# Performance work log

Hardware: AMD Instinct MI355X
Metric: run time of the kernel (lower is better)

Reference implementation:

```python
import math
import jax, jax.numpy as jnp
import numpy as np

B, NP = 256, 3
LAT, TXT, D = 512, 768, 768
NL = 6
DI, DS, DC = 2 * D, 16, 4
DTR = math.ceil(D / 16)
EPS = 1e-5


def _silu(x):
    return x * jax.nn.sigmoid(x)


def _layernorm(x, g, b):
    m = x.mean(-1, keepdims=True)
    v = ((x - m) ** 2).mean(-1, keepdims=True)
    return (x - m) / jnp.sqrt(v + EPS) * g + b


def _mamba(x, in_w, conv_w, conv_b, xproj_w, dt_w, dt_b, Alog, Dp, out_w):
    # x: [B, L, D]; standard Mamba(d_state=16, d_conv=4, expand=2)
    Bb, L, _ = x.shape
    xz = jnp.einsum('bld,ed->ble', x, in_w)          # [B, L, 2*DI]
    u, z = jnp.split(xz, 2, axis=-1)
    # depthwise causal conv (kernel DC, left pad DC-1, truncated to L)
    up = jnp.pad(u, ((0, 0), (DC - 1, 0), (0, 0)))
    uc = conv_b + sum(conv_w[:, k] * up[:, k:k + L, :] for k in range(DC))
    uc = _silu(uc)
    xdbl = jnp.einsum('bld,ed->ble', uc, xproj_w)    # [B, L, DTR+2*DS]
    dt, Bm, Cm = jnp.split(xdbl, [DTR, DTR + DS], axis=-1)
    dt = jax.nn.softplus(jnp.einsum('blr,dr->bld', dt, dt_w) + dt_b)  # [B,L,DI]
    A = -jnp.exp(Alog)                               # [DI, DS]

    def step(h, xs):
        dt_t, B_t, C_t, u_t = xs                     # [B,DI],[B,DS],[B,DS],[B,DI]
        dA = jnp.exp(dt_t[..., None] * A)            # [B,DI,DS]
        h = h * dA + (dt_t * u_t)[..., None] * B_t[:, None, :]
        y = jnp.einsum('bds,bs->bd', h, C_t)
        return h, y

    h0 = jnp.zeros((Bb, DI, DS), x.dtype)
    xs = (dt.transpose(1, 0, 2), Bm.transpose(1, 0, 2),
          Cm.transpose(1, 0, 2), uc.transpose(1, 0, 2))
    _, ys = jax.lax.scan(step, h0, xs)
    y = ys.transpose(1, 0, 2) + Dp * uc
    y = y * _silu(z)
    return jnp.einsum('bld,ed->ble', y, out_w)       # [B, L, D]


def _forward(z_noisy, timestep, text_emb,
             zin_w, zin_b, tin_w, tin_b, time_w, time_b, part_emb,
             local_w, local_b, f_w, f_b, fuse_w, fuse_b, final_w, final_b,
             ln_g, ln_b, m_in_w, m_conv_w, m_conv_b, m_xproj_w, m_dt_w,
             m_dt_b, m_Alog, m_Dp, m_out_w, oln_g, oln_b, zout_w, zout_b):
    z_feat = jnp.einsum('bpl,dl->bpd', z_noisy, zin_w) + zin_b + part_emb
    text_feat = (text_emb @ tin_w.T + tin_b)[:, None]            # [B,1,D]
    half = D // 2
    freqs = jnp.exp(-math.log(10000.0) * jnp.arange(half, dtype=jnp.float32) / half)
    targ = timestep.astype(jnp.float32)[:, None] * freqs
    temb = jnp.concatenate([jnp.cos(targ), jnp.sin(targ)], -1)   # [B,D]
    time_feat = (temb @ time_w.T + time_b)[:, None]              # [B,1,D]
    x = jnp.concatenate([time_feat, text_feat, z_feat], 1)       # [B,5,D]
    # sinusoidal position embedding (first 5 rows of max_len=10 table)
    pos = jnp.arange(5, dtype=jnp.float32)[:, None]
    div = jnp.exp(jnp.arange(0, D, 2, dtype=jnp.float32) * (-math.log(10000.0) / D))
    pe = jnp.zeros((5, D), jnp.float32)
    pe = pe.at[:, 0::2].set(jnp.sin(pos * div)).at[:, 1::2].set(jnp.cos(pos * div))
    x = x + pe[None]
    text_cond = x[:, 1, :]                                       # [B,D]
    for i in range(NL):
        residual = x
        xl = _silu(jnp.einsum('bld,ed->ble', x, local_w[i]) + local_b[i])
        y_rep = jnp.broadcast_to(text_cond[:, None, :], xl.shape)
        yhat = jnp.einsum('bld,ed->ble', jnp.concatenate([xl, y_rep], -1), f_w[i]) + f_b[i]
        y_gate = y_rep * jax.nn.sigmoid(yhat)
        xt = jnp.einsum('bld,ed->ble', jnp.concatenate([xl, y_gate], -1), fuse_w[i]) + fuse_b[i]
        mf = lambda v, d: _mamba(v, m_in_w[i, d], m_conv_w[i, d], m_conv_b[i, d],
                                 m_xproj_w[i, d], m_dt_w[i, d], m_dt_b[i, d],
                                 m_Alog[i, d], m_Dp[i, d], m_out_w[i, d])
        xf = mf(xt, 0)
        xb = jnp.flip(mf(jnp.flip(xt, 1), 1), 1)
        xo = jnp.einsum('bld,ed->ble', jnp.concatenate([xf, xb], -1), final_w[i]) + final_b[i]
        x = _layernorm(xo + residual, ln_g[i], ln_b[i])
    z_out = x[:, 2:, :]                                          # [B,3,D]
    return jnp.einsum('bpd,ld->bpl', _layernorm(z_out, oln_g, oln_b), zout_w) + zout_b


def setup_inputs() -> dict:
    key = jax.random.key(0)
    kit = iter(jax.random.split(key, 40))

    def rn(shape, s=0.02):
        return jax.random.normal(next(kit), shape, jnp.float32) * s

    inp = dict(
        z_noisy=jax.random.normal(next(kit), (B, NP, LAT), jnp.float32),
        text_emb=jax.random.normal(next(kit), (B, TXT), jnp.float32),
        zin_w=rn((D, LAT)), zin_b=jnp.zeros((D,), jnp.float32),
        tin_w=rn((D, TXT)), tin_b=jnp.zeros((D,), jnp.float32),
        time_w=rn((D, D)), time_b=jnp.zeros((D,), jnp.float32),
        part_emb=rn((1, NP, D)),
        local_w=rn((NL, D, D)), local_b=jnp.zeros((NL, D), jnp.float32),
        f_w=rn((NL, D, 2 * D)), f_b=jnp.zeros((NL, D), jnp.float32),
        fuse_w=rn((NL, D, 2 * D)), fuse_b=jnp.zeros((NL, D), jnp.float32),
        final_w=rn((NL, D, 2 * D)), final_b=jnp.zeros((NL, D), jnp.float32),
        ln_g=jnp.ones((NL, D), jnp.float32), ln_b=jnp.zeros((NL, D), jnp.float32),
        m_in_w=rn((NL, 2, 2 * DI, D)),
        m_conv_w=rn((NL, 2, DI, DC), 0.1),
        m_conv_b=jnp.zeros((NL, 2, DI), jnp.float32),
        m_xproj_w=rn((NL, 2, DTR + 2 * DS, DI)),
        m_dt_w=rn((NL, 2, DI, DTR), 0.1),
        m_dt_b=jnp.full((NL, 2, DI), -4.6, jnp.float32),
        m_Alog=jnp.tile(jnp.log(jnp.arange(1, DS + 1, dtype=jnp.float32)), (NL, 2, DI, 1)),
        m_Dp=jnp.ones((NL, 2, DI), jnp.float32),
        m_out_w=rn((NL, 2, D, DI)),
        oln_g=jnp.ones((D,), jnp.float32), oln_b=jnp.zeros((D,), jnp.float32),
        zout_w=rn((LAT, D)), zout_b=jnp.zeros((LAT,), jnp.float32),
        timestep=jax.random.randint(next(kit), (B,), 0, 1000),
    )
    return inp


def reference(z_noisy, text_emb, zin_w, zin_b, tin_w, tin_b, time_w, time_b,
              part_emb, local_w, local_b, f_w, f_b, fuse_w, fuse_b, final_w,
              final_b, ln_g, ln_b, m_in_w, m_conv_w, m_conv_b, m_xproj_w,
              m_dt_w, m_dt_b, m_Alog, m_Dp, m_out_w, oln_g, oln_b, zout_w,
              zout_b, timestep):
    return _forward(z_noisy, timestep, text_emb, zin_w, zin_b, tin_w, tin_b,
                    time_w, time_b, part_emb, local_w, local_b, f_w, f_b,
                    fuse_w, fuse_b, final_w, final_b, ln_g, ln_b, m_in_w,
                    m_conv_w, m_conv_b, m_xproj_w, m_dt_w, m_dt_b, m_Alog,
                    m_Dp, m_out_w, oln_g, oln_b, zout_w, zout_b)
```

## Files before the change

### kernel.cpp

```cpp
#include <hip/hip_runtime.h>
#include <hip/hip_bf16.h>
#include <math.h>

#define B_   256
#define NP_  3
#define LAT_ 512
#define TXT_ 768
#define D_   768
#define NL_  6
#define DI_  1536
#define DS_  16
#define DC_  4
#define DTR_ 48
#define L_   5
#define M_   (B_*L_)
#define EPS_ 1e-5f

#define OB_WBF    0ull
#define OB_XPP    139591680ull
#define OB_TEMB   144310272ull
#define OB_ZNORM  144703488ull
#define OB_XBF    145883136ull
#define OB_TCBF   147849216ull
#define OB_CAT1   148242432ull
#define OB_XTBF   152174592ull
#define OB_XZBF   154140672ull
#define OB_UCY    169869312ull
#define OB_CAT2   177733632ull
#define OB_X      181665792ull
#define OB_TC     185597952ull
#define OB_TCF    186384384ull
#define OB_ZFEAT  187170816ull
#define OB_XO     189530112ull
#define OB_PART   193462272ull

#define WO_LOCAL  0u
#define WO_F      3538944u
#define WO_FUSE   10616832u
#define WO_FINAL  17694720u
#define WO_IN     24772608u
#define WO_OUT    53084160u
#define WO_ZIN    67239936u
#define WO_TIN    67633152u
#define WO_TIME   68222976u
#define WO_ZOUT   68812800u
#define WO_ZNOISY 69206016u
#define WO_TEXT   69599232u
#define WO_END    69795840u

#define CVT_BLOCKS  17040u
#define XPAD_BLOCKS 1152u
#define TEMB_BLOCKS 384u
#define PREP_BLOCKS (CVT_BLOCKS + XPAD_BLOCKS + TEMB_BLOCKS)

typedef __attribute__((ext_vector_type(4))) float floatx4;
typedef __attribute__((ext_vector_type(8))) short short8;
typedef __attribute__((ext_vector_type(8))) unsigned short ushort8v;
typedef __attribute__((ext_vector_type(4))) unsigned short ushort4v;

__device__ __forceinline__ float sigm(float v) { return 1.f / (1.f + expf(-v)); }
__device__ __forceinline__ float softplus(float v) {
    return fmaxf(v, 0.f) + log1pf(expf(-fabsf(v)));
}
__device__ __forceinline__ unsigned short bf16rn(float f) {
    unsigned int u = __builtin_bit_cast(unsigned int, f);
    u = (u + 0x7fffu + ((u >> 16) & 1u)) >> 16;
    return (unsigned short)u;
}
__device__ __forceinline__ float b2f(unsigned short u) {
    unsigned int x = ((unsigned int)u) << 16;
    return __builtin_bit_cast(float, x);
}

template<int N> __device__ __forceinline__ void waitv() {
    asm volatile("s_waitcnt vmcnt(%0)" :: "i"(N) : "memory");
}

struct CvtArgs { const float* s[12]; };

__global__ __launch_bounds__(256) void prep_kernel(
    CvtArgs a, unsigned short* __restrict__ dst,
    const float* __restrict__ xw, unsigned short* __restrict__ xpd,
    const int* __restrict__ ts, unsigned short* __restrict__ temb)
{
    unsigned bid = blockIdx.x;
    if (bid < CVT_BLOCKS) {
        constexpr unsigned ends[12] = {
            3538944u, 10616832u, 17694720u, 24772608u, 53084160u, 67239936u,
            67633152u, 68222976u, 68812800u, 69206016u, 69599232u, 69795840u };
        const unsigned wv = (bid * 256u + threadIdx.x) >> 6;
        const unsigned lane = threadIdx.x & 63u;
        const unsigned wbase = wv * 1024u;
        if (wbase >= WO_END) return;
#pragma unroll
        for (int q = 0; q < 4; ++q) {
            unsigned gbase = wbase + (unsigned)q * 256u;
            if (gbase >= WO_END) return;
            int t = 0;
            while (gbase >= ends[t]) ++t;
            unsigned start = t ? ends[t - 1] : 0u;
            unsigned idx = gbase + lane * 4u;
            floatx4 v = __builtin_nontemporal_load((const floatx4*)(a.s[t] + (idx - start)));
            ushort4v o = { bf16rn(v[0]), bf16rn(v[1]), bf16rn(v[2]), bf16rn(v[3]) };
            __builtin_nontemporal_store(o, (ushort4v*)(dst + idx));
        }
    } else if (bid < CVT_BLOCKS + XPAD_BLOCKS) {
        unsigned i8 = ((bid - CVT_BLOCKS) * 256u + threadIdx.x) * 8u;
        if (i8 >= 12u * 128u * 1536u) return;
        unsigned pi = i8 / (128u * 1536u);
        unsigned rem = i8 - pi * 128u * 1536u;
        unsigned row = rem / 1536u, col = rem - row * 1536u;
        ushort8v o = {0, 0, 0, 0, 0, 0, 0, 0};
        if (row < 80u) {
            const float* s = xw + ((size_t)pi * 80u + row) * 1536u + col;
            floatx4 v0 = __builtin_nontemporal_load((const floatx4*)s);
            floatx4 v1 = __builtin_nontemporal_load((const floatx4*)(s + 4));
            o = ushort8v{ bf16rn(v0[0]), bf16rn(v0[1]), bf16rn(v0[2]), bf16rn(v0[3]),
                          bf16rn(v1[0]), bf16rn(v1[1]), bf16rn(v1[2]), bf16rn(v1[3]) };
        }
        *(ushort8v*)(xpd + i8) = o;
    } else {
        int idx = (bid - CVT_BLOCKS - XPAD_BLOCKS) * 256 + threadIdx.x;
        if (idx >= B_ * 384) return;
        int j = idx % 384, b = idx / 384;
        float f = expf(-logf(10000.f) * (float)j / 384.f);
        float targ = (float)ts[b] * f;
        temb[(size_t)b * D_ + j]       = bf16rn(cosf(targ));
        temb[(size_t)b * D_ + 384 + j] = bf16rn(sinf(targ));
    }
}

template<int BM, int BN, int CD, int DEPTH, int PF>
__global__ __launch_bounds__(256) void gemm_bf16_kernel(
    const unsigned short* __restrict__ A, int lda,
    const unsigned short* __restrict__ W, int wld,
    const float* __restrict__ bias,
    const float* __restrict__ aux0,
    const float* __restrict__ aux1,
    void* __restrict__ Cv, int ldc,
    int M, int N, int K, int epi, int ncap,
    int zsplit, unsigned long long zA, unsigned long long zW, unsigned long long zC)
{
    constexpr int GA = BM / 64;
    constexpr int GB = BN / 64;
    constexpr int LPS = GA + GB;
    constexpr int FRM = BM / 32;
    constexpr int FRN = BN / 32;
    constexpr int BMSK = DEPTH - 1;

    const int z = blockIdx.z;
    const int dirz = z / zsplit, ksz = z - dirz * zsplit;
    A += (unsigned long long)dirz * zA + (unsigned long long)ksz * (unsigned)K;
    W += (unsigned long long)dirz * zW + (unsigned long long)ksz * (unsigned)K;

    __shared__ unsigned short lds[DEPTH][(BM + BN) * 32];

    const int tid = threadIdx.x;
    const int m0 = blockIdx.y * BM, n0 = blockIdx.x * BN;
    const int w = tid >> 6, lane = tid & 63;
    const int wr = w >> 1, wc = w & 1;
    const int lrow = lane & 15;
    const int lk = (lane >> 4) << 3;

    const int rA = tid >> 2, sA = tid & 3;
    const int scA = ((sA ^ ((rA >> 1) & 3)) << 3);
    floatx4 acc[FRM][FRN] = {};

    auto stage = [&](int buf, int k0) {
        unsigned short* base = &lds[buf][0];
#pragma unroll
        for (int i = 0; i < GA; ++i) {
            int t = tid + i * 256;
            int r = t >> 2;
            const unsigned short* src = A + (size_t)(m0 + r) * lda + k0 + scA;
            __builtin_amdgcn_global_load_lds(
                (const __attribute__((address_space(1))) unsigned int*)(const void*)src,
                (__attribute__((address_space(3))) unsigned int*)(void*)(base + i * 2048 + w * 512),
                16, 0, 0);
        }
#pragma unroll
        for (int i = 0; i < GB; ++i) {
            int t = tid + i * 256;
            int r = t >> 2;
            const unsigned short* src = W + (size_t)(n0 + r) * wld + k0 + scA;
            __builtin_amdgcn_global_load_lds(
                (const __attribute__((address_space(1))) unsigned int*)(const void*)src,
                (__attribute__((address_space(3))) unsigned int*)(void*)(base + BM * 32 + i * 2048 + w * 512),
                16, 0, 0);
        }
    };

    const int nt = K >> 5;
#pragma unroll
    for (int s = 0; s < PF; ++s)
        if (s < nt) stage(s, s << 5);

    int offA[FRM], offB[FRN];
#pragma unroll
    for (int i = 0; i < FRM; ++i) {
        int row = wr * (BM / 2) + i * 16 + lrow;
        offA[i] = row * 32 + (lk ^ (((row >> 1) & 3) << 3));
    }
#pragma unroll
    for (int j = 0; j < FRN; ++j) {
        int row = wc * (BN / 2) + j * 16 + lrow;
        offB[j] = BM * 32 + row * 32 + (lk ^ (((row >> 1) & 3) << 3));
    }

    for (int t = 0; t < nt; ++t) {
        int rem = nt - 1 - t;
        if (rem >= PF) { stage((t + PF) & BMSK, (t + PF) << 5); waitv<PF * LPS>(); }
        else if (rem == 5) waitv<5 * LPS>();
        else if (rem == 4) waitv<4 * LPS>();
        else if (rem == 3) waitv<3 * LPS>();
        else if (rem == 2) waitv<2 * LPS>();
        else if (rem == 1) waitv<1 * LPS>();
        else               waitv<0>();
        __builtin_amdgcn_s_barrier();
        const unsigned short* pl = &lds[t & BMSK][0];
        short8 af[FRM], bfv[FRN];
#pragma unroll
        for (int i = 0; i < FRM; ++i) af[i] = *(const short8*)(pl + offA[i]);
#pragma unroll
        for (int j = 0; j < FRN; ++j) bfv[j] = *(const short8*)(pl + offB[j]);
#pragma unroll
        for (int i = 0; i < FRM; ++i)
#pragma unroll
            for (int j = 0; j < FRN; ++j)
                acc[i][j] = __builtin_amdgcn_mfma_f32_16x16x32_bf16(af[i], bfv[j], acc[i][j], 0, 0, 0);
    }

#pragma unroll
    for (int i = 0; i < FRM; ++i) {
        int row0 = m0 + wr * (BM / 2) + i * 16 + (lane >> 4) * 4;
#pragma unroll
        for (int j = 0; j < FRN; ++j) {
            int col = n0 + wc * (BN / 2) + j * 16 + lrow;
            if (col >= ncap) continue;
            float bb = bias ? bias[col] : 0.f;
#pragma unroll
            for (int r = 0; r < 4; ++r) {
                int row = row0 + r;
                float v = acc[i][j][r] + bb;
                if (epi == 1) {
                    v = v * sigm(v);
                } else if (epi == 3) {
                    int b = row / 5;
                    v = acc[i][j][r] + bb + b2f(((const unsigned short*)aux0)[(size_t)b * 768 + col]);
                    v = aux1[(size_t)b * 768 + col] * sigm(v);
                }
                size_t off = (size_t)z * zC + (size_t)row * ldc + col;
                if (CD == 1) ((float*)Cv)[off] = v;
                else         ((unsigned short*)Cv)[off] = bf16rn(v);
            }
        }
    }
}

__global__ void finalize_embed_kernel(float* __restrict__ x,
                                      unsigned short* __restrict__ xbf,
                                      const float* __restrict__ zfeat,
                                      const float* __restrict__ part_emb,
                                      float* __restrict__ tc,
                                      unsigned short* __restrict__ tcbf)
{
    int idx = blockIdx.x * blockDim.x + threadIdx.x;
    if (idx >= B_ * L_ * D_) return;
    int d = idx % D_;
    int bl = idx / D_;
    int l = bl % L_, b = bl / L_;
    float v;
    if (l >= 2) v = zfeat[((size_t)(b * 3 + (l - 2))) * D_ + d] + part_emb[(size_t)(l - 2) * D_ + d];
    else        v = x[idx];
    int j = d >> 1;
    float dv = expf((float)(2 * j) * (-logf(10000.f) / (float)D_));
    float ang = (float)l * dv;
    v += (d & 1) ? cosf(ang) : sinf(ang);
    x[idx] = v;
    xbf[idx] = bf16rn(v);
    if (l == 1) { tc[(size_t)b * D_ + d] = v; tcbf[(size_t)b * D_ + d] = bf16rn(v); }
}

__global__ __launch_bounds__(256) void conv_silu_kernel(
    const unsigned short* __restrict__ xz,
    const float* __restrict__ cw,
    const float* __restrict__ cb,
    unsigned short* __restrict__ ucy)
{
    int idx = blockIdx.x * 256 + threadIdx.x;
    if (idx >= 2 * M_ * DI_ / 8) return;
    int c8 = (idx % (DI_ / 8)) * 8;
    int t2 = idx / (DI_ / 8);
    int bl = t2 % M_, dir = t2 / M_;
    int l = bl % L_, b = bl / L_;

    float acc[8];
    const float* cbp = cb + dir * DI_ + c8;
#pragma unroll
    for (int e = 0; e < 8; ++e) acc[e] = cbp[e];
    floatx4 w[8];
#pragma unroll
    for (int e = 0; e < 8; ++e)
        w[e] = *(const floatx4*)(cw + ((size_t)(dir * DI_ + c8 + e)) * DC_);
#pragma unroll
    for (int k = 0; k < DC_; ++k) {
        int lp = dir ? (l + 3 - k) : (l + k - 3);
        if (lp >= 0 && lp < L_) {
            ushort8v xv = *(const ushort8v*)(xz + ((size_t)(b * L_ + lp)) * 6144 + dir * 3072 + c8);
#pragma unroll
            for (int e = 0; e < 8; ++e) acc[e] = fmaf(w[e][k], b2f(xv[e]), acc[e]);
        }
    }
    ushort8v o;
#pragma unroll
    for (int e = 0; e < 8; ++e) { float v = acc[e]; o[e] = bf16rn(v * sigm(v)); }
    *(ushort8v*)(ucy + (size_t)idx * 8) = o;
}

__global__ __launch_bounds__(256) void dtscan_kernel(
    const float* __restrict__ part,
    unsigned short* ucy,
    const unsigned short* __restrict__ xz,
    const float* __restrict__ dt_w,
    const float* __restrict__ dt_b,
    const float* __restrict__ Alog,
    const float* __restrict__ Dp)
{
    __shared__ float xd[L_][80];
    const int dir = blockIdx.z;
    const int b = blockIdx.y;
    const int ch = blockIdx.x * 256 + threadIdx.x;

    for (int o = threadIdx.x; o < L_ * 80; o += 256) {
        int l = o / 80, n = o - l * 80;
        float s = 0.f;
#pragma unroll
        for (int ks = 0; ks < 8; ++ks)
            s += part[((size_t)(dir * 8 + ks) * M_ + b * L_ + l) * 80 + n];
        xd[l][n] = s;
    }
    __syncthreads();

    const int cg = dir * DI_ + ch;
    float dt[L_];
    const float* wp = dt_w + (size_t)cg * DTR_;
    float dbv = dt_b[cg];
#pragma unroll
    for (int l = 0; l < L_; ++l) {
        float v = dbv;
#pragma unroll
        for (int r = 0; r < DTR_; ++r) v = fmaf(xd[l][r], wp[r], v);
        dt[l] = softplus(v);
    }

    float Aa[DS_], h[DS_];
#pragma unroll
    for (int s = 0; s < DS_; ++s) { Aa[s] = -expf(Alog[(size_t)cg * DS_ + s]); h[s] = 0.f; }
    float Dv = Dp[cg];

#pragma unroll
    for (int t = 0; t < L_; ++t) {
        const int l = dir ? (L_ - 1 - t) : t;
        size_t base = (size_t)(b * L_ + l);
        size_t uoff = ((size_t)dir * M_ + base) * DI_ + ch;
        float dtv = dt[l];
        float ucv = b2f(ucy[uoff]);
        float du = dtv * ucv;
        float y = 0.f;
#pragma unroll
        for (int s = 0; s < DS_; ++s) {
            h[s] = h[s] * expf(dtv * Aa[s]) + du * xd[l][48 + s];
            y = fmaf(h[s], xd[l][64 + s], y);
        }
        float zv = b2f(xz[base * 6144 + dir * 3072 + 1536 + ch]);
        ucy[uoff] = bf16rn((y + Dv * ucv) * (zv * sigm(zv)));
    }
}

__device__ __forceinline__ float block_sum(float v)
{
    __shared__ float sd[4];
#pragma unroll
    for (int o = 1; o < 64; o <<= 1) v += __shfl_xor(v, o, 64);
    int lane = threadIdx.x & 63, wid = threadIdx.x >> 6;
    if (lane == 0) sd[wid] = v;
    __syncthreads();
    v = sd[0] + sd[1] + sd[2] + sd[3];
    __syncthreads();
    return v;
}

__global__ __launch_bounds__(256) void ln_residual_kernel(
    const float* __restrict__ xo, float* __restrict__ x,
    unsigned short* __restrict__ xbf,
    const float* __restrict__ g, const float* __restrict__ bt,
    const float* __restrict__ og, const float* __restrict__ ob,
    unsigned short* __restrict__ znorm, int do_out)
{
    int row = blockIdx.x;
    const float* pa = xo + (size_t)row * D_;
    float* px = x + (size_t)row * D_;
    float v[3];
    float s = 0.f;
#pragma unroll
    for (int i = 0; i < 3; ++i) { int d = threadIdx.x + 256 * i; v[i] = pa[d] + px[d]; s += v[i]; }
    float mean = block_sum(s) * (1.f / (float)D_);
    float sq = 0.f;
#pragma unroll
    for (int i = 0; i < 3; ++i) { float t = v[i] - mean; sq += t * t; }
    float var = block_sum(sq) * (1.f / (float)D_);
    float inv = rsqrtf(var + EPS_);
    float o[3];
#pragma unroll
    for (int i = 0; i < 3; ++i) {
        int d = threadIdx.x + 256 * i;
        o[i] = (v[i] - mean) * inv * g[d] + bt[d];
        px[d] = o[i];
        xbf[(size_t)row * D_ + d] = bf16rn(o[i]);
    }
    int l = row % L_;
    if (do_out && l >= 2) {
        int b = row / L_;
        float s2 = o[0] + o[1] + o[2];
        float mean2 = block_sum(s2) * (1.f / (float)D_);
        float sq2 = 0.f;
#pragma unroll
        for (int i = 0; i < 3; ++i) { float t = o[i] - mean2; sq2 += t * t; }
        float var2 = block_sum(sq2) * (1.f / (float)D_);
        float inv2 = rsqrtf(var2 + EPS_);
#pragma unroll
        for (int i = 0; i < 3; ++i) {
            int d = threadIdx.x + 256 * i;
            znorm[((size_t)(b * 3 + (l - 2))) * D_ + d] = bf16rn((o[i] - mean2) * inv2 * og[d] + ob[d]);
        }
    }
}

extern "C" void kernel_launch(void* const* d_in, const int* in_sizes, int n_in,
                              void* d_out, int out_size, void* d_ws, size_t ws_size,
                              hipStream_t stream)
{
    const float* z_noisy  = (const float*)d_in[0];
    const float* text_emb = (const float*)d_in[1];
    const float* zin_b    = (const float*)d_in[3];
    const float* tin_b    = (const float*)d_in[5];
    const float* time_b   = (const float*)d_in[7];
    const float* part_emb = (const float*)d_in[8];
    const float* local_b  = (const float*)d_in[10];
    const float* f_b      = (const float*)d_in[12];
    const float* fuse_b   = (const float*)d_in[14];
    const float* final_b  = (const float*)d_in[16];
    const float* ln_g     = (const float*)d_in[17];
    const float* ln_b     = (const float*)d_in[18];
    const float* m_conv_w = (const float*)d_in[20];
    const float* m_conv_b = (const float*)d_in[21];
    const float* m_xproj_w= (const float*)d_in[22];
    const float* m_dt_w   = (const float*)d_in[23];
    const float* m_dt_b   = (const float*)d_in[24];
    const float* m_Alog   = (const float*)d_in[25];
    const float* m_Dp     = (const float*)d_in[26];
    const float* oln_g    = (const float*)d_in[28];
    const float* oln_b    = (const float*)d_in[29];
    const float* zout_b   = (const float*)d_in[31];
    const int*   timestep = (const int*)d_in[32];

    char* wsb = (char*)d_ws;
    unsigned short* wbf   = (unsigned short*)(wsb + OB_WBF);
    unsigned short* xpp   = (unsigned short*)(wsb + OB_XPP);
    unsigned short* tembb = (unsigned short*)(wsb + OB_TEMB);
    unsigned short* znormb= (unsigned short*)(wsb + OB_ZNORM);
    unsigned short* xbf   = (unsigned short*)(wsb + OB_XBF);
    unsigned short* tcbf  = (unsigned short*)(wsb + OB_TCBF);
    unsigned short* cat1b = (unsigned short*)(wsb + OB_CAT1);
    unsigned short* xtbf  = (unsigned short*)(wsb + OB_XTBF);
    unsigned short* xzbf  = (unsigned short*)(wsb + OB_XZBF);
    unsigned short* ucy   = (unsigned short*)(wsb + OB_UCY);
    unsigned short* cat2b = (unsigned short*)(wsb + OB_CAT2);
    float* x     = (float*)(wsb + OB_X);
    float* tc    = (float*)(wsb + OB_TC);
    float* zfeat = (float*)(wsb + OB_ZFEAT);
    unsigned short* tcf6 = (unsigned short*)(wsb + OB_ZFEAT);
    float* xo    = (float*)(wsb + OB_XO);
    float* part  = (float*)(wsb + OB_PART);

    unsigned short* local_bf = wbf + WO_LOCAL;
    unsigned short* f_bf     = wbf + WO_F;
    unsigned short* fuse_bf  = wbf + WO_FUSE;
    unsigned short* final_bf = wbf + WO_FINAL;
    unsigned short* in_bf    = wbf + WO_IN;
    unsigned short* out_bf   = wbf + WO_OUT;
    unsigned short* zin_bf   = wbf + WO_ZIN;
    unsigned short* tin_bf   = wbf + WO_TIN;
    unsigned short* time_bf  = wbf + WO_TIME;
    unsigned short* zout_bf  = wbf + WO_ZOUT;
    unsigned short* znz_bf   = wbf + WO_ZNOISY;
    unsigned short* text_bf  = wbf + WO_TEXT;

    auto ew = [&](int n) { return dim3((n + 255) / 256); };

    CvtArgs ca;
    ca.s[0] = (const float*)d_in[9];
    ca.s[1] = (const float*)d_in[11];
    ca.s[2] = (const float*)d_in[13];
    ca.s[3] = (const float*)d_in[15];
    ca.s[4] = (const float*)d_in[19];
    ca.s[5] = (const float*)d_in[27];
    ca.s[6] = (const float*)d_in[2];
    ca.s[7] = (const float*)d_in[4];
    ca.s[8] = (const float*)d_in[6];
    ca.s[9] = (const float*)d_in[30];
    ca.s[10] = z_noisy;
    ca.s[11] = text_emb;
    hipLaunchKernelGGL(prep_kernel, dim3(PREP_BLOCKS), dim3(256), 0, stream,
                       ca, wbf, m_xproj_w, xpp, timestep, tembb);

    auto g64d = [&](const unsigned short* A, int lda, const unsigned short* W, int wld,
                    const float* bias, const float* a0, const float* a1,
                    void* C, int ldc, int Mm, int Nn, int Kk, int epi, int ncap, int cd,
                    int gz, int zsplit, unsigned long long zA, unsigned long long zW,
                    unsigned long long zC) {
        dim3 g(Nn / 64, Mm / 64, gz);
        if (cd == 1)
            gemm_bf16_kernel<64, 64, 1, 8, 6><<<g, dim3(256), 0, stream>>>(
                A, lda, W, wld, bias, a0, a1, C, ldc, Mm, Nn, Kk, epi, ncap, zsplit, zA, zW, zC);
        else
            gemm_bf16_kernel<64, 64, 0, 8, 6><<<g, dim3(256), 0, stream>>>(
                A, lda, W, wld, bias, a0, a1, C, ldc, Mm, Nn, Kk, epi, ncap, zsplit, zA, zW, zC);
    };
    auto g64s = [&](const unsigned short* A, int lda, const unsigned short* W, int wld,
                    const float* bias, const float* a0, const float* a1,
                    void* C, int ldc, int Mm, int Nn, int Kk, int epi, int ncap, int cd,
                    int gz, int zsplit, unsigned long long zA, unsigned long long zW,
                    unsigned long long zC) {
        dim3 g(Nn / 64, Mm / 64, gz);
        if (cd == 1)
            gemm_bf16_kernel<64, 64, 1, 4, 2><<<g, dim3(256), 0, stream>>>(
                A, lda, W, wld, bias, a0, a1, C, ldc, Mm, Nn, Kk, epi, ncap, zsplit, zA, zW, zC);
        else
            gemm_bf16_kernel<64, 64, 0, 4, 2><<<g, dim3(256), 0, stream>>>(
                A, lda, W, wld, bias, a0, a1, C, ldc, Mm, Nn, Kk, epi, ncap, zsplit, zA, zW, zC);
    };

    g64d(tembb, D_, time_bf, D_, time_b, nullptr, nullptr, x, L_ * D_, B_, D_, D_, 0, D_, 1,
         1, 1, 0, 0, 0);
    g64d(text_bf, TXT_, tin_bf, TXT_, tin_b, nullptr, nullptr, x + D_, L_ * D_, B_, D_, TXT_, 0, D_, 1,
         1, 1, 0, 0, 0);
    g64d(znz_bf, LAT_, zin_bf, LAT_, zin_b, nullptr, nullptr, zfeat, D_, B_ * NP_, D_, LAT_, 0, D_, 1,
         1, 1, 0, 0, 0);
    hipLaunchKernelGGL(finalize_embed_kernel, ew(B_ * L_ * D_), dim3(256), 0, stream,
                       x, xbf, zfeat, part_emb, tc, tcbf);

    g64d(tcbf, D_, f_bf + D_, 2 * D_, nullptr, nullptr, nullptr,
         tcf6, D_, B_, D_, D_, 0, D_, 0,
         6, 1, 0ull, (unsigned long long)D_ * 2 * D_, (unsigned long long)B_ * D_);

    for (int i = 0; i < NL_; ++i) {
        g64d(xbf, D_, local_bf + (size_t)i * D_ * D_, D_, local_b + (size_t)i * D_,
             nullptr, nullptr, cat1b, 2 * D_, M_, D_, D_, 1, D_, 0, 1, 1, 0, 0, 0);
        g64d(cat1b, 2 * D_, f_bf + (size_t)i * D_ * 2 * D_, 2 * D_, f_b + (size_t)i * D_,
             (const float*)(tcf6 + (size_t)i * B_ * D_), tc,
             cat1b + D_, 2 * D_, M_, D_, D_, 3, D_, 0, 1, 1, 0, 0, 0);
        g64d(cat1b, 2 * D_, fuse_bf + (size_t)i * D_ * 2 * D_, 2 * D_, fuse_b + (size_t)i * D_,
             nullptr, nullptr, xtbf, D_, M_, D_, 2 * D_, 0, D_, 0, 1, 1, 0, 0, 0);

        {
            dim3 g(6144 / 128, M_ / 128, 1);
            gemm_bf16_kernel<128, 128, 0, 4, 2><<<g, dim3(256), 0, stream>>>(
                xtbf, D_, in_bf + (size_t)i * 4718592ull, D_, nullptr, nullptr, nullptr,
                xzbf, 6144, M_, 6144, D_, 0, 6144, 1, 0, 0, 0);
        }
        hipLaunchKernelGGL(conv_silu_kernel, dim3(2 * M_ * DI_ / 8 / 256), dim3(256), 0, stream,
                           xzbf, m_conv_w + (size_t)i * 2 * DI_ * DC_,
                           m_conv_b + (size_t)i * 2 * DI_, ucy);
        g64s(ucy, DI_, xpp + (size_t)i * 2 * 128 * DI_, DI_, nullptr, nullptr, nullptr,
             part, 80, M_, 128, 192, 0, 80, 1,
             16, 8, (unsigned long long)M_ * DI_, (unsigned long long)128 * DI_,
             (unsigned long long)M_ * 80);
        hipLaunchKernelGGL(dtscan_kernel, dim3(DI_ / 256, B_, 2), dim3(256), 0, stream,
                           part, ucy, xzbf,
                           m_dt_w + (size_t)i * 2 * DI_ * DTR_, m_dt_b + (size_t)i * 2 * DI_,
                           m_Alog + (size_t)i * 2 * DI_ * DS_, m_Dp + (size_t)i * 2 * DI_);
        {
            dim3 g(D_ / 64, M_ / 128, 2);
            gemm_bf16_kernel<128, 64, 0, 8, 6><<<g, dim3(256), 0, stream>>>(
                ucy, DI_, out_bf + (size_t)i * 2 * D_ * DI_, DI_, nullptr, nullptr, nullptr,
                cat2b, 2 * D_, M_, D_, DI_, 0, D_,
                1, (unsigned long long)M_ * DI_, (unsigned long long)D_ * DI_, 768ull);
        }
        g64d(cat2b, 2 * D_, final_bf + (size_t)i * D_ * 2 * D_, 2 * D_, final_b + (size_t)i * D_,
             nullptr, nullptr, xo, D_, M_, D_, 2 * D_, 0, D_, 1, 1, 1, 0, 0, 0);
        hipLaunchKernelGGL(ln_residual_kernel, dim3(M_), dim3(256), 0, stream,
                           xo, x, xbf, ln_g + (size_t)i * D_, ln_b + (size_t)i * D_,
                           oln_g, oln_b, znormb, (i == NL_ - 1) ? 1 : 0);
    }

    g64d(znormb, D_, zout_bf, D_, zout_b, nullptr, nullptr,
         (float*)d_out, LAT_, B_ * NP_, LAT_, D_, 0, LAT_, 1, 1, 1, 0, 0, 0);
}
```

Measured before the change: 1.156 ms.

## Fuse conv-SiLU, x_proj, and selective scan into one Mamba kernel

Replaces three launches per layer (depthwise conv+SiLU, split-K x_proj GEMM with partial sums, and dt/scan) with one kernel per (batch, direction). The conv output is kept in LDS, x_proj is computed there with fp32 weights via wave reductions, and the scan reads the conv output from LDS. This removes the ucy and partial-sum round trips through global memory, the bf16 padded x_proj weight prep, and two launches. In exchange x_proj no longer uses MFMA, each block rereads the full 80x1536 weight slice from global/L2, and the grid is only 512 blocks of 512 threads with a large LDS footprint, which may lower occupancy.

```diff
diff --git a/kernel.cpp b/kernel.cpp
--- a/kernel.cpp
+++ b/kernel.cpp
@@ -17,7 +17,6 @@
 #define EPS_ 1e-5f
 
 #define OB_WBF    0ull
-#define OB_XPP    139591680ull
 #define OB_TEMB   144310272ull
 #define OB_ZNORM  144703488ull
 #define OB_XBF    145883136ull
@@ -29,10 +28,8 @@
 #define OB_CAT2   177733632ull
 #define OB_X      181665792ull
 #define OB_TC     185597952ull
-#define OB_TCF    186384384ull
 #define OB_ZFEAT  187170816ull
 #define OB_XO     189530112ull
-#define OB_PART   193462272ull
 
 #define WO_LOCAL  0u
 #define WO_F      3538944u
@@ -49,9 +46,8 @@
 #define WO_END    69795840u
 
 #define CVT_BLOCKS  17040u
-#define XPAD_BLOCKS 1152u
 #define TEMB_BLOCKS 384u
-#define PREP_BLOCKS (CVT_BLOCKS + XPAD_BLOCKS + TEMB_BLOCKS)
+#define PREP_BLOCKS (CVT_BLOCKS + TEMB_BLOCKS)
 
 typedef __attribute__((ext_vector_type(4))) float floatx4;
 typedef __attribute__((ext_vector_type(8))) short short8;
@@ -80,7 +76,6 @@
 
 __global__ __launch_bounds__(256) void prep_kernel(
     CvtArgs a, unsigned short* __restrict__ dst,
-    const float* __restrict__ xw, unsigned short* __restrict__ xpd,
     const int* __restrict__ ts, unsigned short* __restrict__ temb)
 {
     unsigned bid = blockIdx.x;
@@ -104,23 +99,8 @@
             ushort4v o = { bf16rn(v[0]), bf16rn(v[1]), bf16rn(v[2]), bf16rn(v[3]) };
             __builtin_nontemporal_store(o, (ushort4v*)(dst + idx));
         }
-    } else if (bid < CVT_BLOCKS + XPAD_BLOCKS) {
-        unsigned i8 = ((bid - CVT_BLOCKS) * 256u + threadIdx.x) * 8u;
-        if (i8 >= 12u * 128u * 1536u) return;
-        unsigned pi = i8 / (128u * 1536u);
-        unsigned rem = i8 - pi * 128u * 1536u;
-        unsigned row = rem / 1536u, col = rem - row * 1536u;
-        ushort8v o = {0, 0, 0, 0, 0, 0, 0, 0};
-        if (row < 80u) {
-            const float* s = xw + ((size_t)pi * 80u + row) * 1536u + col;
-            floatx4 v0 = __builtin_nontemporal_load((const floatx4*)s);
-            floatx4 v1 = __builtin_nontemporal_load((const floatx4*)(s + 4));
-            o = ushort8v{ bf16rn(v0[0]), bf16rn(v0[1]), bf16rn(v0[2]), bf16rn(v0[3]),
-                          bf16rn(v1[0]), bf16rn(v1[1]), bf16rn(v1[2]), bf16rn(v1[3]) };
-        }
-        *(ushort8v*)(xpd + i8) = o;
     } else {
-        int idx = (bid - CVT_BLOCKS - XPAD_BLOCKS) * 256 + threadIdx.x;
+        int idx = (bid - CVT_BLOCKS) * 256 + threadIdx.x;
         if (idx >= B_ * 384) return;
         int j = idx % 384, b = idx / 384;
         float f = expf(-logf(10000.f) * (float)j / 384.f);
@@ -281,99 +261,111 @@
     if (l == 1) { tc[(size_t)b * D_ + d] = v; tcbf[(size_t)b * D_ + d] = bf16rn(v); }
 }
 
-__global__ __launch_bounds__(256) void conv_silu_kernel(
+__global__ __launch_bounds__(512) void mamba_fused_kernel(
     const unsigned short* __restrict__ xz,
+    const float* __restrict__ xw,
     const float* __restrict__ cw,
     const float* __restrict__ cb,
-    unsigned short* __restrict__ ucy)
-{
-    int idx = blockIdx.x * 256 + threadIdx.x;
-    if (idx >= 2 * M_ * DI_ / 8) return;
-    int c8 = (idx % (DI_ / 8)) * 8;
-    int t2 = idx / (DI_ / 8);
-    int bl = t2 % M_, dir = t2 / M_;
-    int l = bl % L_, b = bl / L_;
-
-    float acc[8];
-    const float* cbp = cb + dir * DI_ + c8;
-#pragma unroll
-    for (int e = 0; e < 8; ++e) acc[e] = cbp[e];
-    floatx4 w[8];
-#pragma unroll
-    for (int e = 0; e < 8; ++e)
-        w[e] = *(const floatx4*)(cw + ((size_t)(dir * DI_ + c8 + e)) * DC_);
-#pragma unroll
-    for (int k = 0; k < DC_; ++k) {
-        int lp = dir ? (l + 3 - k) : (l + k - 3);
-        if (lp >= 0 && lp < L_) {
-            ushort8v xv = *(const ushort8v*)(xz + ((size_t)(b * L_ + lp)) * 6144 + dir * 3072 + c8);
-#pragma unroll
-            for (int e = 0; e < 8; ++e) acc[e] = fmaf(w[e][k], b2f(xv[e]), acc[e]);
-        }
-    }
-    ushort8v o;
-#pragma unroll
-    for (int e = 0; e < 8; ++e) { float v = acc[e]; o[e] = bf16rn(v * sigm(v)); }
-    *(ushort8v*)(ucy + (size_t)idx * 8) = o;
-}
-
-__global__ __launch_bounds__(256) void dtscan_kernel(
-    const float* __restrict__ part,
-    unsigned short* ucy,
-    const unsigned short* __restrict__ xz,
     const float* __restrict__ dt_w,
     const float* __restrict__ dt_b,
     const float* __restrict__ Alog,
-    const float* __restrict__ Dp)
-{
+    const float* __restrict__ Dp,
+    unsigned short* __restrict__ ucy)
+{
+    __shared__ unsigned short uc[L_][DI_];
     __shared__ float xd[L_][80];
-    const int dir = blockIdx.z;
-    const int b = blockIdx.y;
-    const int ch = blockIdx.x * 256 + threadIdx.x;
-
-    for (int o = threadIdx.x; o < L_ * 80; o += 256) {
-        int l = o / 80, n = o - l * 80;
-        float s = 0.f;
-#pragma unroll
-        for (int ks = 0; ks < 8; ++ks)
-            s += part[((size_t)(dir * 8 + ks) * M_ + b * L_ + l) * 80 + n];
-        xd[l][n] = s;
+
+    const int b = blockIdx.x;
+    const int dir = blockIdx.y;
+    const int tid = threadIdx.x;
+
+    for (int u = tid; u < L_ * DI_ / 8; u += 512) {
+        int l = u / (DI_ / 8);
+        int c8 = (u % (DI_ / 8)) * 8;
+        float acc[8];
+        const float* cbp = cb + dir * DI_ + c8;
+#pragma unroll
+        for (int e = 0; e < 8; ++e) acc[e] = cbp[e];
+        floatx4 w[8];
+#pragma unroll
+        for (int e = 0; e < 8; ++e)
+            w[e] = *(const floatx4*)(cw + ((size_t)(dir * DI_ + c8 + e)) * DC_);
+#pragma unroll
+        for (int k = 0; k < DC_; ++k) {
+            int lp = dir ? (l + 3 - k) : (l + k - 3);
+            if (lp >= 0 && lp < L_) {
+                ushort8v xv = *(const ushort8v*)(xz + ((size_t)(b * L_ + lp)) * 6144 + dir * 3072 + c8);
+#pragma unroll
+                for (int e = 0; e < 8; ++e) acc[e] = fmaf(w[e][k], b2f(xv[e]), acc[e]);
+            }
+        }
+        ushort8v o;
+#pragma unroll
+        for (int e = 0; e < 8; ++e) { float v = acc[e]; o[e] = bf16rn(v * sigm(v)); }
+        *(ushort8v*)(&uc[l][c8]) = o;
     }
     __syncthreads();
 
-    const int cg = dir * DI_ + ch;
-    float dt[L_];
-    const float* wp = dt_w + (size_t)cg * DTR_;
-    float dbv = dt_b[cg];
-#pragma unroll
-    for (int l = 0; l < L_; ++l) {
-        float v = dbv;
-#pragma unroll
-        for (int r = 0; r < DTR_; ++r) v = fmaf(xd[l][r], wp[r], v);
-        dt[l] = softplus(v);
-    }
-
-    float Aa[DS_], h[DS_];
-#pragma unroll
-    for (int s = 0; s < DS_; ++s) { Aa[s] = -expf(Alog[(size_t)cg * DS_ + s]); h[s] = 0.f; }
-    float Dv = Dp[cg];
-
-#pragma unroll
-    for (int t = 0; t < L_; ++t) {
-        const int l = dir ? (L_ - 1 - t) : t;
-        size_t base = (size_t)(b * L_ + l);
-        size_t uoff = ((size_t)dir * M_ + base) * DI_ + ch;
-        float dtv = dt[l];
-        float ucv = b2f(ucy[uoff]);
-        float du = dtv * ucv;
-        float y = 0.f;
-#pragma unroll
-        for (int s = 0; s < DS_; ++s) {
-            h[s] = h[s] * expf(dtv * Aa[s]) + du * xd[l][48 + s];
-            y = fmaf(h[s], xd[l][64 + s], y);
-        }
-        float zv = b2f(xz[base * 6144 + dir * 3072 + 1536 + ch]);
-        ucy[uoff] = bf16rn((y + Dv * ucv) * (zv * sigm(zv)));
+    {
+        const int wv = tid >> 6, lane = tid & 63;
+        for (int n = wv; n < 80; n += 8) {
+            const float* wp = xw + ((size_t)dir * 80 + n) * DI_;
+            floatx4 wreg[6];
+#pragma unroll
+            for (int j = 0; j < 6; ++j) wreg[j] = *(const floatx4*)(wp + j * 256 + lane * 4);
+#pragma unroll
+            for (int l = 0; l < L_; ++l) {
+                float s = 0.f;
+#pragma unroll
+                for (int j = 0; j < 6; ++j) {
+                    ushort4v uv = *(const ushort4v*)(&uc[l][j * 256 + lane * 4]);
+                    s = fmaf(b2f(uv[0]), wreg[j][0], s);
+                    s = fmaf(b2f(uv[1]), wreg[j][1], s);
+                    s = fmaf(b2f(uv[2]), wreg[j][2], s);
+                    s = fmaf(b2f(uv[3]), wreg[j][3], s);
+                }
+#pragma unroll
+                for (int d = 1; d < 64; d <<= 1) s += __shfl_xor(s, d, 64);
+                if (lane == 0) xd[l][n] = s;
+            }
+        }
+    }
+    __syncthreads();
+
+#pragma unroll
+    for (int j3 = 0; j3 < 3; ++j3) {
+        int ch = tid + 512 * j3;
+        const int cg = dir * DI_ + ch;
+        float dt[L_];
+        const float* wp = dt_w + (size_t)cg * DTR_;
+        float dbv = dt_b[cg];
+#pragma unroll
+        for (int l = 0; l < L_; ++l) {
+            float v = dbv;
+#pragma unroll
+            for (int r = 0; r < DTR_; ++r) v = fmaf(xd[l][r], wp[r], v);
+            dt[l] = softplus(v);
+        }
+        float Aa[DS_], h[DS_];
+#pragma unroll
+        for (int s = 0; s < DS_; ++s) { Aa[s] = -expf(Alog[(size_t)cg * DS_ + s]); h[s] = 0.f; }
+        float Dv = Dp[cg];
+#pragma unroll
+        for (int t = 0; t < L_; ++t) {
+            const int l = dir ? (L_ - 1 - t) : t;
+            size_t base = (size_t)(b * L_ + l);
+            float dtv = dt[l];
+            float ucv = b2f(uc[l][ch]);
+            float du = dtv * ucv;
+            float y = 0.f;
+#pragma unroll
+            for (int s = 0; s < DS_; ++s) {
+                h[s] = h[s] * expf(dtv * Aa[s]) + du * xd[l][48 + s];
+                y = fmaf(h[s], xd[l][64 + s], y);
+            }
+            float zv = b2f(xz[base * 6144 + dir * 3072 + 1536 + ch]);
+            ucy[((size_t)dir * M_ + base) * DI_ + ch] = bf16rn((y + Dv * ucv) * (zv * sigm(zv)));
+        }
     }
 }
 
@@ -466,7 +458,6 @@
 
     char* wsb = (char*)d_ws;
     unsigned short* wbf   = (unsigned short*)(wsb + OB_WBF);
-    unsigned short* xpp   = (unsigned short*)(wsb + OB_XPP);
     unsigned short* tembb = (unsigned short*)(wsb + OB_TEMB);
     unsigned short* znormb= (unsigned short*)(wsb + OB_ZNORM);
     unsigned short* xbf   = (unsigned short*)(wsb + OB_XBF);
@@ -481,7 +472,6 @@
     float* zfeat = (float*)(wsb + OB_ZFEAT);
     unsigned short* tcf6 = (unsigned short*)(wsb + OB_ZFEAT);
     float* xo    = (float*)(wsb + OB_XO);
-    float* part  = (float*)(wsb + OB_PART);
 
     unsigned short* local_bf = wbf + WO_LOCAL;
     unsigned short* f_bf     = wbf + WO_F;
@@ -512,7 +502,7 @@
     ca.s[10] = z_noisy;
     ca.s[11] = text_emb;
     hipLaunchKernelGGL(prep_kernel, dim3(PREP_BLOCKS), dim3(256), 0, stream,
-                       ca, wbf, m_xproj_w, xpp, timestep, tembb);
+                       ca, wbf, timestep, tembb);
 
     auto g64d = [&](const unsigned short* A, int lda, const unsigned short* W, int wld,
                     const float* bias, const float* a0, const float* a1,
@@ -527,19 +517,6 @@
             gemm_bf16_kernel<64, 64, 0, 8, 6><<<g, dim3(256), 0, stream>>>(
                 A, lda, W, wld, bias, a0, a1, C, ldc, Mm, Nn, Kk, epi, ncap, zsplit, zA, zW, zC);
     };
-    auto g64s = [&](const unsigned short* A, int lda, const unsigned short* W, int wld,
-                    const float* bias, const float* a0, const float* a1,
-                    void* C, int ldc, int Mm, int Nn, int Kk, int epi, int ncap, int cd,
-                    int gz, int zsplit, unsigned long long zA, unsigned long long zW,
-                    unsigned long long zC) {
-        dim3 g(Nn / 64, Mm / 64, gz);
-        if (cd == 1)
-            gemm_bf16_kernel<64, 64, 1, 4, 2><<<g, dim3(256), 0, stream>>>(
-                A, lda, W, wld, bias, a0, a1, C, ldc, Mm, Nn, Kk, epi, ncap, zsplit, zA, zW, zC);
-        else
-            gemm_bf16_kernel<64, 64, 0, 4, 2><<<g, dim3(256), 0, stream>>>(
-                A, lda, W, wld, bias, a0, a1, C, ldc, Mm, Nn, Kk, epi, ncap, zsplit, zA, zW, zC);
-    };
 
     g64d(tembb, D_, time_bf, D_, time_b, nullptr, nullptr, x, L_ * D_, B_, D_, D_, 0, D_, 1,
          1, 1, 0, 0, 0);
@@ -569,17 +546,16 @@
                 xtbf, D_, in_bf + (size_t)i * 4718592ull, D_, nullptr, nullptr, nullptr,
                 xzbf, 6144, M_, 6144, D_, 0, 6144, 1, 0, 0, 0);
         }
-        hipLaunchKernelGGL(conv_silu_kernel, dim3(2 * M_ * DI_ / 8 / 256), dim3(256), 0, stream,
-                           xzbf, m_conv_w + (size_t)i * 2 * DI_ * DC_,
-                           m_conv_b + (size_t)i * 2 * DI_, ucy);
-        g64s(ucy, DI_, xpp + (size_t)i * 2 * 128 * DI_, DI_, nullptr, nullptr, nullptr,
-             part, 80, M_, 128, 192, 0, 80, 1,
-             16, 8, (unsigned long long)M_ * DI_, (unsigned long long)128 * DI_,
-             (unsigned long long)M_ * 80);
-        hipLaunchKernelGGL(dtscan_kernel, dim3(DI_ / 256, B_, 2), dim3(256), 0, stream,
-                           part, ucy, xzbf,
-                           m_dt_w + (size_t)i * 2 * DI_ * DTR_, m_dt_b + (size_t)i * 2 * DI_,
-                           m_Alog + (size_t)i * 2 * DI_ * DS_, m_Dp + (size_t)i * 2 * DI_);
+        hipLaunchKernelGGL(mamba_fused_kernel, dim3(B_, 2), dim3(512), 0, stream,
+                           xzbf,
+                           m_xproj_w + (size_t)i * 2 * 80 * DI_,
+                           m_conv_w + (size_t)i * 2 * DI_ * DC_,
+                           m_conv_b + (size_t)i * 2 * DI_,
+                           m_dt_w + (size_t)i * 2 * DI_ * DTR_,
+                           m_dt_b + (size_t)i * 2 * DI_,
+                           m_Alog + (size_t)i * 2 * DI_ * DS_,
+                           m_Dp + (size_t)i * 2 * DI_,
+                           ucy);
         {
             dim3 g(D_ / 64, M_ / 128, 2);
             gemm_bf16_kernel<128, 64, 0, 8, 6><<<g, dim3(256), 0, stream>>>(
```

Measured after the change: 1.433 ms. 24.0% more time.
